# Kernel optimization log

Measured on AMD Instinct MI355X. Metric: run time of the kernel, lower is better.

## Reference

```python
import jax, jax.numpy as jnp
import numpy as np

N_NODES = 50000
N_EDGES = 800000
IN_FEATS = 128
HIDDEN = 128
OUT_LEN = 128


def setup_inputs() -> dict:
    key = jax.random.key(0)
    ks = jax.random.split(key, 8)
    feat = jax.random.normal(ks[0], (N_NODES, IN_FEATS), dtype=jnp.float32)
    # Glorot-ish init for weights, zeros for bias (DGL GraphConv default)
    def w(k, fi, fo):
        return jax.random.normal(k, (fi, fo), dtype=jnp.float32) / np.sqrt(fi)
    W1 = w(ks[1], IN_FEATS, HIDDEN)
    W2 = w(ks[2], HIDDEN, HIDDEN)
    W3 = w(ks[3], HIDDEN, OUT_LEN)
    b1 = jnp.zeros((HIDDEN,), jnp.float32)
    b2 = jnp.zeros((HIDDEN,), jnp.float32)
    b3 = jnp.zeros((OUT_LEN,), jnp.float32)
    src = jax.random.randint(ks[4], (N_EDGES,), 0, N_NODES, dtype=jnp.int32)
    dst = jax.random.randint(ks[5], (N_EDGES,), 0, N_NODES, dtype=jnp.int32)
    return {"feat": feat, "W1": W1, "b1": b1, "W2": W2, "b2": b2,
            "W3": W3, "b3": b3, "src": src, "dst": dst}


def _degree_norm(idx, n):
    # degree counts, clamped to min 1 (DGL behavior), then ^{-1/2}
    deg = jax.ops.segment_sum(jnp.ones_like(idx, dtype=jnp.float32), idx,
                              num_segments=n)
    return jax.lax.rsqrt(jnp.maximum(deg, 1.0))


def _graph_conv(x, W, b, src, dst, out_norm, in_norm):
    # DGL GraphConv, norm='both':
    # h = D_dst^{-1/2} * segsum_dst( D_src^{-1/2} * x[src] ) @ W + b
    h = x * out_norm[:, None]
    m = jax.ops.segment_sum(h[src], dst, num_segments=x.shape[0])  # [N, d]
    m = m * in_norm[:, None]
    return m @ W + b


def reference(feat, W1, b1, W2, b2, W3, b3, src, dst):
    out_norm = _degree_norm(src, feat.shape[0])  # out-degree norm (source)
    in_norm = _degree_norm(dst, feat.shape[0])   # in-degree norm (dest)
    h = jax.nn.relu(_graph_conv(feat, W1, b1, src, dst, out_norm, in_norm))
    h = jax.nn.relu(_graph_conv(h, W2, b2, src, dst, out_norm, in_norm))
    h = _graph_conv(h, W3, b3, src, dst, out_norm, in_norm)
    # single graph: mean_nodes == mean over all nodes, then squeeze -> [out_len]
    return jnp.mean(h, axis=0)
```

## Files before the change

### kernel.cpp

```cpp
#include <hip/hip_runtime.h>

#define N_NODES 50000
#define N_EDGES 800000
#define F 128
#define SCAN_NB 49
#define CH 64
#define EPC (N_EDGES / CH)
#define HALF 25000
#define QTR 12500
#define BSTRIDE 17
#define AGG_NB (N_NODES / 4)
#define GB ((N_NODES + 63) / 64)

typedef __bf16 bf16x8 __attribute__((ext_vector_type(8)));
typedef float  f32x4  __attribute__((ext_vector_type(4)));
typedef float  f32x2  __attribute__((ext_vector_type(2)));

__device__ inline unsigned short f2bf(float f) {
    unsigned u = __float_as_uint(f);
    u += 0x7FFF + ((u >> 16) & 1);
    return (unsigned short)(u >> 16);
}
__device__ inline unsigned packbf2(float a, float b) {
    return (unsigned)f2bf(a) | ((unsigned)f2bf(b) << 16);
}

__device__ inline void fp8x8_to_f32(uint2 u, float* f) {
    f32x2 v0 = __builtin_amdgcn_cvt_pk_f32_fp8(u.x, false);
    f32x2 v1 = __builtin_amdgcn_cvt_pk_f32_fp8(u.x, true);
    f32x2 v2 = __builtin_amdgcn_cvt_pk_f32_fp8(u.y, false);
    f32x2 v3 = __builtin_amdgcn_cvt_pk_f32_fp8(u.y, true);
    f[0] = v0.x; f[1] = v0.y; f[2] = v1.x; f[3] = v1.y;
    f[4] = v2.x; f[5] = v2.y; f[6] = v3.x; f[7] = v3.y;
}
__device__ inline unsigned f32x4_to_fp8(float a, float b, float c, float d) {
    unsigned r = __builtin_amdgcn_cvt_pk_fp8_f32(a, b, 0, false);
    r = __builtin_amdgcn_cvt_pk_fp8_f32(c, d, r, true);
    return r;
}

__global__ __launch_bounds__(1024) void hist_kernel(const int* __restrict__ src,
                                                    const int* __restrict__ dst,
                                                    unsigned char* __restrict__ Hs8,
                                                    unsigned char* __restrict__ Hd8,
                                                    int* __restrict__ bsump) {
    __shared__ unsigned hist[HALF / 4];
    int bx = blockIdx.x;
    int c = bx >> 2, t = bx & 1, h = (bx >> 1) & 1;
    const int* ids = t ? dst : src;
    unsigned char* H = t ? Hd8 : Hs8;
    int base = h * HALF;
    for (int j = threadIdx.x; j < HALF / 4; j += 1024) hist[j] = 0;
    __syncthreads();
    int e0 = c * EPC;
    for (int e = e0 + threadIdx.x; e < e0 + EPC; e += 1024) {
        int id = ids[e] - base;
        if ((unsigned)id < (unsigned)HALF)
            atomicAdd(&hist[id >> 2], 1u << ((id & 3) * 8));
    }
    __syncthreads();
    unsigned* Hw = (unsigned*)(H + (size_t)c * N_NODES + base);
    for (int j = threadIdx.x; j < HALF / 4; j += 1024) Hw[j] = hist[j];
    if (t) {
        int w = threadIdx.x >> 6, lane = threadIdx.x & 63;
        for (int r = w; r < SCAN_NB; r += 16) {
            int gi0 = max(r * 1024, base);
            int gi1 = min(r * 1024 + 1024, base + HALF);
            int s = 0;
            for (int li = gi0 - base + lane; li < gi1 - base; li += 64)
                s += (hist[li >> 2] >> ((li & 3) * 8)) & 255;
#pragma unroll
            for (int off = 32; off; off >>= 1) s += __shfl_down(s, off);
            if (lane == 0) bsump[(c * 2 + h) * SCAN_NB + r] = s;
        }
    }
}

__global__ __launch_bounds__(1024) void scanC_kernel(const unsigned char* __restrict__ Hs8,
                                                     const unsigned char* __restrict__ Hd8,
                                                     const int* __restrict__ bsump,
                                                     float* __restrict__ onorm,
                                                     float* __restrict__ inorm,
                                                     int* __restrict__ rowst,
                                                     unsigned char* __restrict__ P8) {
    __shared__ int wsum[16];
    __shared__ int tot[SCAN_NB];
    int t = threadIdx.x, lane = t & 63, w = t >> 6;
    int i = blockIdx.x * 1024 + t;
    if (t < SCAN_NB) {
        int s = 0;
        for (int p = 0; p < 2 * CH; p++) s += bsump[p * SCAN_NB + t];
        tot[t] = s;
    }
    int dd = 0;
    if (i < N_NODES) {
        int ds = 0, run = 0;
        for (int c = 0; c < CH; c++) {
            size_t o = (size_t)c * N_NODES + i;
            ds += Hs8[o];
            P8[o] = (unsigned char)run;
            run += Hd8[o];
        }
        dd = run;
        onorm[i] = rsqrtf(fmaxf((float)ds, 1.0f));
        inorm[i] = rsqrtf(fmaxf((float)dd, 1.0f));
    }
    int v = dd, incl = v;
#pragma unroll
    for (int off = 1; off < 64; off <<= 1) {
        int u = __shfl_up(incl, off);
        if (lane >= off) incl += u;
    }
    if (lane == 63) wsum[w] = incl;
    __syncthreads();
    if (t == 0) {
        int s = 0;
        for (int r = 0; r < (int)blockIdx.x; r++) s += tot[r];
#pragma unroll
        for (int k = 0; k < 16; k++) { int x = wsum[k]; wsum[k] = s; s += x; }
    }
    __syncthreads();
    incl += wsum[w];
    if (i < N_NODES) {
        rowst[i] = incl - v;
        if (i == N_NODES - 1) rowst[N_NODES] = incl;
    }
}

__global__ __launch_bounds__(1024) void tqsc_kernel(const int* __restrict__ src,
                                                    const int* __restrict__ dst,
                                                    const float* __restrict__ inorm,
                                                    float* __restrict__ Tq,
                                                    const int* __restrict__ rowst,
                                                    const unsigned char* __restrict__ P8,
                                                    int* __restrict__ esrc,
                                                    const float* __restrict__ feat,
                                                    const float* __restrict__ onorm,
                                                    uint2* __restrict__ xq,
                                                    const float* __restrict__ W1,
                                                    const float* __restrict__ W2,
                                                    unsigned short* __restrict__ Wt) {
    __shared__ float a[QTR];
    __shared__ int cur[QTR];
    int bx = blockIdx.x;
    int c = bx >> 2, q = bx & 3;
    int base = q * QTR;
    int e0 = c * EPC;

    for (int j = threadIdx.x; j < QTR; j += 1024) {
        a[j] = 0.0f;
        cur[j] = rowst[base + j] + (int)P8[(size_t)c * N_NODES + base + j];
    }
    __syncthreads();

    for (int e = e0 + threadIdx.x; e < e0 + EPC; e += 1024) {
        int s = src[e], d = dst[e];
        int sq = s - base;
        if ((unsigned)sq < (unsigned)QTR)
            atomicAdd(&a[sq], inorm[d]);
        int dq = d - base;
        if ((unsigned)dq < (unsigned)QTR) {
            int pos = atomicAdd(&cur[dq], 1);
            esrc[pos] = s;
        }
    }
    __syncthreads();
    for (int j = threadIdx.x; j < QTR; j += 1024)
        Tq[(size_t)c * N_NODES + base + j] = a[j];

    int T = gridDim.x * 1024;
    int id0 = bx * 1024 + threadIdx.x;
    for (int i = id0; i < N_NODES * F / 8; i += T) {
        float w = onorm[i >> 4];
        const float4* xv = (const float4*)feat;
        float4 v0 = xv[i * 2], v1 = xv[i * 2 + 1];
        uint2 o;
        o.x = f32x4_to_fp8(v0.x * w, v0.y * w, v0.z * w, v0.w * w);
        o.y = f32x4_to_fp8(v1.x * w, v1.y * w, v1.z * w, v1.w * w);
        xq[i] = o;
    }
    for (int i = id0; i < 2 * F * F; i += T) {
        int wi = i >> 14, rem = i & 16383;
        int n = rem >> 7, k = rem & 127;
        const float* W = wi ? W2 : W1;
        Wt[(size_t)wi * F * F + (size_t)n * F + k] = f2bf(W[k * F + n]);
    }
}

template <int QT>
__global__ __launch_bounds__(256) void agg_csr_kernel(const uint2* __restrict__ xq,
                                                      uint4* __restrict__ mb,
                                                      const int* __restrict__ rowst,
                                                      const int* __restrict__ esrc,
                                                      const float* __restrict__ inorm,
                                                      const float* __restrict__ Tq,
                                                      float* __restrict__ qt) {
    int w = threadIdx.x >> 6;
    int lane = threadIdx.x & 63;
    int g = lane >> 4, t = lane & 15;
    int row = blockIdx.x * 4 + w;
    int beg = __builtin_amdgcn_readfirstlane(rowst[row]);
    int end = __builtin_amdgcn_readfirstlane(rowst[row + 1]);
    float acc[8];
#pragma unroll
    for (int k = 0; k < 8; k++) acc[k] = 0.0f;

    for (int e = beg; e < end; e += 16) {
        int ea = min(e + g,      end - 1);
        int eb = min(e + 4 + g,  end - 1);
        int ec = min(e + 8 + g,  end - 1);
        int ed = min(e + 12 + g, end - 1);
        int sa = esrc[ea], sb = esrc[eb], sc = esrc[ec], sd = esrc[ed];
        uint2 ua = xq[(size_t)sa * 16 + t];
        uint2 ub = xq[(size_t)sb * 16 + t];
        uint2 uc = xq[(size_t)sc * 16 + t];
        uint2 ud = xq[(size_t)sd * 16 + t];
        float wa = (e + g      < end) ? 1.0f : 0.0f;
        float wb = (e + 4 + g  < end) ? 1.0f : 0.0f;
        float wc = (e + 8 + g  < end) ? 1.0f : 0.0f;
        float wd = (e + 12 + g < end) ? 1.0f : 0.0f;
        float fa[8], fb[8], fc[8], fd[8];
        fp8x8_to_f32(ua, fa); fp8x8_to_f32(ub, fb);
        fp8x8_to_f32(uc, fc); fp8x8_to_f32(ud, fd);
#pragma unroll
        for (int k = 0; k < 8; k++)
            acc[k] += fa[k] * wa + fb[k] * wb + fc[k] * wc + fd[k] * wd;
    }
#pragma unroll
    for (int k = 0; k < 8; k++) {
        acc[k] += __shfl_xor(acc[k], 16, 64);
        acc[k] += __shfl_xor(acc[k], 32, 64);
    }
    if (g == 0) {
        float inw = inorm[row];
        uint4 o;
        o.x = packbf2(acc[0] * inw, acc[1] * inw);
        o.y = packbf2(acc[2] * inw, acc[3] * inw);
        o.z = packbf2(acc[4] * inw, acc[5] * inw);
        o.w = packbf2(acc[6] * inw, acc[7] * inw);
        mb[(size_t)row * 16 + t] = o;
    }
    if (QT) {
        int i = blockIdx.x * 256 + threadIdx.x;
        if (i < N_NODES) {
            float s = 0.0f;
            for (int c = 0; c < CH; c++) s += Tq[(size_t)c * N_NODES + i];
            qt[i] = s;
        }
    }
}

template <int FINAL>
__global__ __launch_bounds__(256) void mfma_gemm_kernel(const unsigned short* __restrict__ A,
                                                        const unsigned short* __restrict__ Wt,
                                                        const float* __restrict__ bias,
                                                        const float* __restrict__ onorm,
                                                        unsigned char* __restrict__ Y8,
                                                        const float* __restrict__ qt,
                                                        float* __restrict__ part2) {
    __shared__ uint4 sB[F * BSTRIDE];
    __shared__ float sPf[4][F];
    int tid = threadIdx.x;
    int w = tid >> 6;
    int lane = tid & 63;
    int quad = lane >> 4, r16 = lane & 15;
    int row0 = blockIdx.x * 64 + w * 16;

    int arow = min(row0 + r16, N_NODES - 1);
    const uint4* Arow = (const uint4*)(A + (size_t)arow * F);
    uint4 a[4];
#pragma unroll
    for (int kk = 0; kk < 4; kk++) a[kk] = Arow[kk * 4 + quad];

    const uint4* G = (const uint4*)Wt;
    for (int j = tid; j < F * 16; j += 256)
        sB[(j >> 4) * BSTRIDE + (j & 15)] = G[j];

    f32x4 acc[8];
#pragma unroll
    for (int t = 0; t < 8; t++) acc[t] = (f32x4){0.f, 0.f, 0.f, 0.f};
    __syncthreads();

#pragma unroll
    for (int kk = 0; kk < 4; kk++) {
        bf16x8 av = __builtin_bit_cast(bf16x8, a[kk]);
#pragma unroll
        for (int t = 0; t < 8; t++) {
            bf16x8 bv = __builtin_bit_cast(bf16x8,
                sB[(t * 16 + r16) * BSTRIDE + kk * 4 + quad]);
            acc[t] = __builtin_amdgcn_mfma_f32_16x16x32_bf16(av, bv, acc[t], 0, 0, 0);
        }
    }

    float rw[4];
#pragma unroll
    for (int reg = 0; reg < 4; reg++) {
        int row = row0 + quad * 4 + reg;
        rw[reg] = (row < N_NODES) ? (FINAL ? qt[row] * onorm[row] : onorm[row]) : 0.0f;
    }

    if (!FINAL) {
#pragma unroll
        for (int t = 0; t < 8; t++) {
            int col = t * 16 + r16;
            float bb = bias[col];
#pragma unroll
            for (int reg = 0; reg < 4; reg++) {
                int row = row0 + quad * 4 + reg;
                if (row < N_NODES) {
                    float v = fmaxf(acc[t][reg] + bb, 0.0f) * rw[reg];
                    unsigned p = __builtin_amdgcn_cvt_pk_fp8_f32(v, v, 0, false);
                    Y8[(size_t)row * F + col] = (unsigned char)(p & 0xFF);
                }
            }
        }
    } else {
#pragma unroll
        for (int t = 0; t < 8; t++) {
            int col = t * 16 + r16;
            float bb = bias[col];
            float p = 0.0f;
#pragma unroll
            for (int reg = 0; reg < 4; reg++)
                p += fmaxf(acc[t][reg] + bb, 0.0f) * rw[reg];
            p += __shfl_xor(p, 16, 64);
            p += __shfl_xor(p, 32, 64);
            if (quad == 0) sPf[w][col] = p;
        }
        __syncthreads();
        if (tid < F)
            part2[(size_t)blockIdx.x * F + tid] =
                sPf[0][tid] + sPf[1][tid] + sPf[2][tid] + sPf[3][tid];
    }
}

__global__ __launch_bounds__(1024) void final_kernel(const float* __restrict__ part2,
                                                     const float* __restrict__ W3,
                                                     const float* __restrict__ b3,
                                                     float* __restrict__ out) {
    __shared__ float sc[8][F];
    int tid = threadIdx.x;
    int col = tid & 127, sl = tid >> 7;
    float acc = 0.0f;
    for (int b = sl; b < GB; b += 8) acc += part2[(size_t)b * F + col];
    sc[sl][col] = acc;
    __syncthreads();
    if (tid < F) {
        float s = 0.0f;
#pragma unroll
        for (int k = 0; k < 8; k++) s += sc[k][tid];
        sc[0][tid] = s * (1.0f / (float)N_NODES);
    }
    __syncthreads();
    if (tid < F) {
        float o = b3[tid];
        for (int k = 0; k < F; k++) o += sc[0][k] * W3[k * F + tid];
        out[tid] = o;
    }
}

extern "C" void kernel_launch(void* const* d_in, const int* in_sizes, int n_in,
                              void* d_out, int out_size, void* d_ws, size_t ws_size,
                              hipStream_t stream) {
    const float* feat = (const float*)d_in[0];
    const float* W1   = (const float*)d_in[1];
    const float* b1   = (const float*)d_in[2];
    const float* W2   = (const float*)d_in[3];
    const float* b2   = (const float*)d_in[4];
    const float* W3   = (const float*)d_in[5];
    const float* b3   = (const float*)d_in[6];
    const int*   src  = (const int*)d_in[7];
    const int*   dst  = (const int*)d_in[8];
    float* out = (float*)d_out;

    char* ws = (char*)d_ws;
    size_t off = 0;
    uint4* mb    = (uint4*)(ws + off); off += (size_t)N_NODES * F * 2;
    float* Tq    = (float*)(ws + off); off += (size_t)CH * N_NODES * 4;
    uint2* xq    = (uint2*)(ws + off); off += (size_t)N_NODES * F;
    uint2* hq    = (uint2*)(ws + off); off += (size_t)N_NODES * F;
    unsigned char* Hs8 = (unsigned char*)(ws + off); off += (size_t)CH * N_NODES;
    unsigned char* Hd8 = (unsigned char*)(ws + off); off += (size_t)CH * N_NODES;
    unsigned char* P8  = (unsigned char*)(ws + off); off += (size_t)CH * N_NODES;
    int*   esrc  = (int*)  (ws + off); off += (size_t)N_EDGES * 4;
    unsigned short* Wt = (unsigned short*)(ws + off); off += 2 * F * F * 2;
    float* part2 = (float*)(ws + off); off += (size_t)GB * F * 4;
    float* onorm = (float*)(ws + off); off += N_NODES * 4;
    float* inorm = (float*)(ws + off); off += N_NODES * 4;
    float* qt    = (float*)(ws + off); off += N_NODES * 4;
    int*   rowst = (int*)  (ws + off); off += (N_NODES + 1) * 4;
    int*   bsump = (int*)  (ws + off); off += 2 * CH * SCAN_NB * 4;

    hist_kernel<<<4 * CH, 1024, 0, stream>>>(src, dst, Hs8, Hd8, bsump);
    scanC_kernel<<<SCAN_NB, 1024, 0, stream>>>(Hs8, Hd8, bsump, onorm, inorm,
                                               rowst, P8);
    tqsc_kernel<<<4 * CH, 1024, 0, stream>>>(src, dst, inorm, Tq, rowst, P8,
                                             esrc, feat, onorm, xq, W1, W2, Wt);

    agg_csr_kernel<1><<<AGG_NB, 256, 0, stream>>>(xq, mb, rowst, esrc, inorm, Tq, qt);
    mfma_gemm_kernel<0><<<GB, 256, 0, stream>>>((const unsigned short*)mb, Wt, b1,
                                                onorm, (unsigned char*)hq, qt, part2);
    agg_csr_kernel<0><<<AGG_NB, 256, 0, stream>>>(hq, mb, rowst, esrc, inorm, Tq, qt);
    mfma_gemm_kernel<1><<<GB, 256, 0, stream>>>((const unsigned short*)mb, Wt + F * F,
                                                b2, onorm, (unsigned char*)hq, qt, part2);
    final_kernel<<<1, 1024, 0, stream>>>(part2, W3, b3, out);
}
```

Before: 217.4 us.

## Atomically accumulate qt and fold final reduction into last GEMM block

Replaces the per-chunk Tq buffer (64×N floats) with atomic adds into a single qt accumulator in the scatter kernel, which removes the 64-way column reduction that agg_csr did in layer 1. The final kernel is also removed: the last GEMM accumulates column sums into a global buffer with atomics and uses a ticket counter so the last block computes the W3 projection. This saves a launch and a large buffer write/read. In exchange it adds global atomic contention and makes float summation order nondeterministic.

```diff
diff --git a/kernel.cpp b/kernel.cpp
--- a/kernel.cpp
+++ b/kernel.cpp
@@ -82,11 +82,18 @@
                                                      float* __restrict__ onorm,
                                                      float* __restrict__ inorm,
                                                      int* __restrict__ rowst,
-                                                     unsigned char* __restrict__ P8) {
+                                                     unsigned char* __restrict__ P8,
+                                                     float* __restrict__ qtacc,
+                                                     float* __restrict__ cacc,
+                                                     int* __restrict__ ticket) {
     __shared__ int wsum[16];
     __shared__ int tot[SCAN_NB];
     int t = threadIdx.x, lane = t & 63, w = t >> 6;
     int i = blockIdx.x * 1024 + t;
+    if (blockIdx.x == 0) {
+        if (t < F) cacc[t] = 0.0f;
+        if (t == F) *ticket = 0;
+    }
     if (t < SCAN_NB) {
         int s = 0;
         for (int p = 0; p < 2 * CH; p++) s += bsump[p * SCAN_NB + t];
@@ -104,6 +111,7 @@
         dd = run;
         onorm[i] = rsqrtf(fmaxf((float)ds, 1.0f));
         inorm[i] = rsqrtf(fmaxf((float)dd, 1.0f));
+        qtacc[i] = 0.0f;
     }
     int v = dd, incl = v;
 #pragma unroll
@@ -130,7 +138,7 @@
 __global__ __launch_bounds__(1024) void tqsc_kernel(const int* __restrict__ src,
                                                     const int* __restrict__ dst,
                                                     const float* __restrict__ inorm,
-                                                    float* __restrict__ Tq,
+                                                    float* __restrict__ qtacc,
                                                     const int* __restrict__ rowst,
                                                     const unsigned char* __restrict__ P8,
                                                     int* __restrict__ esrc,
@@ -165,8 +173,10 @@
         }
     }
     __syncthreads();
-    for (int j = threadIdx.x; j < QTR; j += 1024)
-        Tq[(size_t)c * N_NODES + base + j] = a[j];
+    for (int j = threadIdx.x; j < QTR; j += 1024) {
+        float v = a[j];
+        if (v != 0.0f) atomicAdd(&qtacc[base + j], v);
+    }
 
     int T = gridDim.x * 1024;
     int id0 = bx * 1024 + threadIdx.x;
@@ -187,14 +197,11 @@
     }
 }
 
-template <int QT>
 __global__ __launch_bounds__(256) void agg_csr_kernel(const uint2* __restrict__ xq,
                                                       uint4* __restrict__ mb,
                                                       const int* __restrict__ rowst,
                                                       const int* __restrict__ esrc,
-                                                      const float* __restrict__ inorm,
-                                                      const float* __restrict__ Tq,
-                                                      float* __restrict__ qt) {
+                                                      const float* __restrict__ inorm) {
     int w = threadIdx.x >> 6;
     int lane = threadIdx.x & 63;
     int g = lane >> 4, t = lane & 15;
@@ -240,14 +247,6 @@
         o.w = packbf2(acc[6] * inw, acc[7] * inw);
         mb[(size_t)row * 16 + t] = o;
     }
-    if (QT) {
-        int i = blockIdx.x * 256 + threadIdx.x;
-        if (i < N_NODES) {
-            float s = 0.0f;
-            for (int c = 0; c < CH; c++) s += Tq[(size_t)c * N_NODES + i];
-            qt[i] = s;
-        }
-    }
 }
 
 template <int FINAL>
@@ -257,9 +256,14 @@
                                                         const float* __restrict__ onorm,
                                                         unsigned char* __restrict__ Y8,
                                                         const float* __restrict__ qt,
-                                                        float* __restrict__ part2) {
+                                                        float* __restrict__ cacc,
+                                                        int* __restrict__ ticket,
+                                                        const float* __restrict__ W3,
+                                                        const float* __restrict__ b3,
+                                                        float* __restrict__ out) {
     __shared__ uint4 sB[F * BSTRIDE];
     __shared__ float sPf[4][F];
+    __shared__ int lastFlag;
     int tid = threadIdx.x;
     int w = tid >> 6;
     int lane = tid & 63;
@@ -329,33 +333,23 @@
         }
         __syncthreads();
         if (tid < F)
-            part2[(size_t)blockIdx.x * F + tid] =
-                sPf[0][tid] + sPf[1][tid] + sPf[2][tid] + sPf[3][tid];
-    }
-}
-
-__global__ __launch_bounds__(1024) void final_kernel(const float* __restrict__ part2,
-                                                     const float* __restrict__ W3,
-                                                     const float* __restrict__ b3,
-                                                     float* __restrict__ out) {
-    __shared__ float sc[8][F];
-    int tid = threadIdx.x;
-    int col = tid & 127, sl = tid >> 7;
-    float acc = 0.0f;
-    for (int b = sl; b < GB; b += 8) acc += part2[(size_t)b * F + col];
-    sc[sl][col] = acc;
-    __syncthreads();
-    if (tid < F) {
-        float s = 0.0f;
-#pragma unroll
-        for (int k = 0; k < 8; k++) s += sc[k][tid];
-        sc[0][tid] = s * (1.0f / (float)N_NODES);
-    }
-    __syncthreads();
-    if (tid < F) {
-        float o = b3[tid];
-        for (int k = 0; k < F; k++) o += sc[0][k] * W3[k * F + tid];
-        out[tid] = o;
+            atomicAdd(&cacc[tid],
+                      sPf[0][tid] + sPf[1][tid] + sPf[2][tid] + sPf[3][tid]);
+        __threadfence();
+        if (tid == 0) lastFlag = (atomicAdd(ticket, 1) == GB - 1);
+        __syncthreads();
+        if (lastFlag) {
+            if (tid < F) {
+                float c = atomicAdd(&cacc[tid], 0.0f);
+                sPf[0][tid] = c * (1.0f / (float)N_NODES);
+            }
+            __syncthreads();
+            if (tid < F) {
+                float o = b3[tid];
+                for (int k = 0; k < F; k++) o += sPf[0][k] * W3[k * F + tid];
+                out[tid] = o;
+            }
+        }
     }
 }
 
@@ -376,7 +370,6 @@
     char* ws = (char*)d_ws;
     size_t off = 0;
     uint4* mb    = (uint4*)(ws + off); off += (size_t)N_NODES * F * 2;
-    float* Tq    = (float*)(ws + off); off += (size_t)CH * N_NODES * 4;
     uint2* xq    = (uint2*)(ws + off); off += (size_t)N_NODES * F;
     uint2* hq    = (uint2*)(ws + off); off += (size_t)N_NODES * F;
     unsigned char* Hs8 = (unsigned char*)(ws + off); off += (size_t)CH * N_NODES;
@@ -384,24 +377,26 @@
     unsigned char* P8  = (unsigned char*)(ws + off); off += (size_t)CH * N_NODES;
     int*   esrc  = (int*)  (ws + off); off += (size_t)N_EDGES * 4;
     unsigned short* Wt = (unsigned short*)(ws + off); off += 2 * F * F * 2;
-    float* part2 = (float*)(ws + off); off += (size_t)GB * F * 4;
     float* onorm = (float*)(ws + off); off += N_NODES * 4;
     float* inorm = (float*)(ws + off); off += N_NODES * 4;
-    float* qt    = (float*)(ws + off); off += N_NODES * 4;
+    float* qtacc = (float*)(ws + off); off += N_NODES * 4;
     int*   rowst = (int*)  (ws + off); off += (N_NODES + 1) * 4;
     int*   bsump = (int*)  (ws + off); off += 2 * CH * SCAN_NB * 4;
+    float* cacc  = (float*)(ws + off); off += F * 4;
+    int*   ticket= (int*)  (ws + off); off += 16;
 
     hist_kernel<<<4 * CH, 1024, 0, stream>>>(src, dst, Hs8, Hd8, bsump);
     scanC_kernel<<<SCAN_NB, 1024, 0, stream>>>(Hs8, Hd8, bsump, onorm, inorm,
-                                               rowst, P8);
-    tqsc_kernel<<<4 * CH, 1024, 0, stream>>>(src, dst, inorm, Tq, rowst, P8,
+                                               rowst, P8, qtacc, cacc, ticket);
+    tqsc_kernel<<<4 * CH, 1024, 0, stream>>>(src, dst, inorm, qtacc, rowst, P8,
                                              esrc, feat, onorm, xq, W1, W2, Wt);
 
-    agg_csr_kernel<1><<<AGG_NB, 256, 0, stream>>>(xq, mb, rowst, esrc, inorm, Tq, qt);
+    agg_csr_kernel<<<AGG_NB, 256, 0, stream>>>(xq, mb, rowst, esrc, inorm);
     mfma_gemm_kernel<0><<<GB, 256, 0, stream>>>((const unsigned short*)mb, Wt, b1,
-                                                onorm, (unsigned char*)hq, qt, part2);
-    agg_csr_kernel<0><<<AGG_NB, 256, 0, stream>>>(hq, mb, rowst, esrc, inorm, Tq, qt);
+                                                onorm, (unsigned char*)hq, qtacc,
+                                                cacc, ticket, W3, b3, out);
+    agg_csr_kernel<<<AGG_NB, 256, 0, stream>>>(hq, mb, rowst, esrc, inorm);
     mfma_gemm_kernel<1><<<GB, 256, 0, stream>>>((const unsigned short*)mb, Wt + F * F,
-                                                b2, onorm, (unsigned char*)hq, qt, part2);
-    final_kernel<<<1, 1024, 0, stream>>>(part2, W3, b3, out);
-}
+                                                b2, onorm, (unsigned char*)hq, qtacc,
+                                                cacc, ticket, W3, b3, out);
+}
```

Result: slower. 255.4 us (+17.5%).
